# Kernel optimization log

Hardware: AMD Instinct MI355X
Metric: run time of the kernel (lower is better)

The kernel has to match this reference:

```python
import jax, jax.numpy as jnp
import numpy as np

N, E, G, D, H = 20000, 320000, 64, 56, 256


def setup_inputs() -> dict:
    key = jax.random.key(0)
    ks = jax.random.split(key, 12)
    inp = {}
    inp["x"] = jax.random.normal(ks[0], (N, D), jnp.float32)
    inp["edge_index"] = jax.random.randint(ks[1], (2, E), 0, N)
    inp["batch"] = jnp.sort(jax.random.randint(ks[2], (N,), 0, G))
    dims = [D, H, H]
    i = 3
    for l, d_in in enumerate(dims):
        inp[f"w1_{l}"] = jax.random.normal(ks[i], (2 * d_in, H), jnp.float32) * 0.05; i += 1
        inp[f"b1_{l}"] = jnp.zeros((H,), jnp.float32)
        inp[f"w2_{l}"] = jax.random.normal(ks[i], (H, H), jnp.float32) * 0.05; i += 1
        inp[f"b2_{l}"] = jnp.zeros((H,), jnp.float32)
    inp["wc1"] = jax.random.normal(ks[9], (2 * H, H), jnp.float32) * 0.05
    inp["bc1"] = jnp.zeros((H,), jnp.float32)
    inp["wc2"] = jax.random.normal(ks[10], (H, 64), jnp.float32) * 0.05
    inp["bc2"] = jnp.zeros((64,), jnp.float32)
    inp["wc3"] = jax.random.normal(ks[11], (64, 1), jnp.float32) * 0.05
    inp["bc3"] = jnp.zeros((1,), jnp.float32)
    return inp


def _edge_conv(x, src, dst, w1, b1, w2, b2):
    # PyG EdgeConv: message = mlp(cat([x_i, x_j - x_i])), max-aggregated at target i
    xi = x[dst]                       # [E, d]
    xj = x[src]                       # [E, d]
    h = jnp.concatenate([xi, xj - xi], axis=-1)  # [E, 2d]
    h = jax.nn.relu(h @ w1 + b1) @ w2 + b2       # [E, H]
    agg = jax.ops.segment_max(h, dst, num_segments=N)  # [N, H]
    return jnp.where(jnp.isfinite(agg), agg, 0.0)      # nodes with no in-edges -> 0


def reference(x, edge_index, batch,
              w1_0, b1_0, w2_0, b2_0,
              w1_1, b1_1, w2_1, b2_1,
              w1_2, b1_2, w2_2, b2_2,
              wc1, bc1, wc2, bc2, wc3, bc3):
    src, dst = edge_index[0], edge_index[1]
    for (w1, b1, w2, b2) in [(w1_0, b1_0, w2_0, b2_0),
                             (w1_1, b1_1, w2_1, b2_1),
                             (w1_2, b1_2, w2_2, b2_2)]:
        x = _edge_conv(x, src, dst, w1, b1, w2, b2)
        # dropout is identity at eval time
    # global mean / max pooling over graphs
    counts = jax.ops.segment_sum(jnp.ones((N,), x.dtype), batch, num_segments=G)
    x_mean = jax.ops.segment_sum(x, batch, num_segments=G) / jnp.maximum(counts, 1.0)[:, None]
    x_max = jax.ops.segment_max(x, batch, num_segments=G)
    x_max = jnp.where(jnp.isfinite(x_max), x_max, 0.0)
    g = jnp.concatenate([x_mean, x_max], axis=1)  # [G, 2H]
    h = jax.nn.relu(g @ wc1 + bc1)
    h = jax.nn.relu(h @ wc2 + bc2)
    out = h @ wc3 + bc3                            # [G, 1]
    return out.squeeze(-1)
```

## Files before the change

kernel.cpp:

```cpp
#include <hip/hip_runtime.h>

#define N_NODES 20000
#define N_EDGES 320000
#define N_GRAPHS 64
#define HID 256
#define EB 64
#define NB (N_EDGES / EB)
#define NBK 48

typedef __attribute__((ext_vector_type(8))) short bf16x8;
typedef __attribute__((ext_vector_type(4))) float f32x4;

__device__ __forceinline__ unsigned short bf16_rne(float f) {
  unsigned u = __float_as_uint(f);
  u = u + 0x7FFFu + ((u >> 16) & 1u);
  return (unsigned short)(u >> 16);
}

__device__ __forceinline__ unsigned int enc_f32(float v) {
  unsigned int bits = __float_as_uint(v);
  return (bits & 0x80000000u) ? ~bits : (bits | 0x80000000u);
}

__device__ __forceinline__ float dec_u32(unsigned int u) {
  if (u == 0u) return 0.f;
  unsigned int bits = (u & 0x80000000u) ? (u ^ 0x80000000u) : ~u;
  return __uint_as_float(bits);
}

__global__ __launch_bounds__(256) void hist_kernel(const int* __restrict__ ei,
                                                   int* __restrict__ deg) {
  int e = blockIdx.x * 256 + threadIdx.x;
  if (e < N_EDGES) atomicAdd(&deg[ei[N_EDGES + e]], 1);
}

__global__ __launch_bounds__(256) void scan_kernel(const int* __restrict__ deg,
                                                   int* __restrict__ cursor) {
  __shared__ int part[256];
  const int tid = threadIdx.x;
  const int CH = (N_NODES + 255) / 256;
  int s = tid * CH;
  int e = s + CH; if (e > N_NODES) e = N_NODES; if (s > N_NODES) s = N_NODES;
  int sum = 0;
  for (int i = s; i < e; i++) sum += deg[i];
  part[tid] = sum;
  __syncthreads();
  for (int off = 1; off < 256; off <<= 1) {
    int v = (tid >= off) ? part[tid - off] : 0;
    __syncthreads();
    part[tid] += v;
    __syncthreads();
  }
  int prefix = (tid == 0) ? 0 : part[tid - 1];
  for (int i = s; i < e; i++) {
    cursor[i] = prefix;
    prefix += deg[i];
  }
}

__global__ __launch_bounds__(256) void scatter_kernel(const int* __restrict__ ei,
                                                      int* __restrict__ cursor,
                                                      int* __restrict__ csr_src,
                                                      int* __restrict__ csr_dst) {
  int e = blockIdx.x * 256 + threadIdx.x;
  if (e < N_EDGES) {
    int s = ei[e], d = ei[N_EDGES + e];
    int pos = atomicAdd(&cursor[d], 1);
    csr_src[pos] = s;
    csr_dst[pos] = d;
  }
}

__global__ __launch_bounds__(256) void prep_weights_kernel(
    const float* __restrict__ w2_0, const float* __restrict__ w2_1,
    const float* __restrict__ w2_2,
    const float* __restrict__ w1_1, const float* __restrict__ w1_2,
    unsigned short* __restrict__ w2t_hi, unsigned short* __restrict__ w2t_lo,
    unsigned short* __restrict__ w1t_hi, unsigned short* __restrict__ w1t_lo) {
  const int b = blockIdx.x;
  const int k = threadIdx.x;
  if (b < 768) {
    int l = b >> 8, j = b & 255;
    const float* w2 = (l == 0) ? w2_0 : ((l == 1) ? w2_1 : w2_2);
    float v = w2[k * HID + j];
    unsigned short hi = bf16_rne(v);
    float rem = v - __uint_as_float(((unsigned)hi) << 16);
    w2t_hi[((size_t)l * HID + j) * HID + k] = hi;
    w2t_lo[((size_t)l * HID + j) * HID + k] = bf16_rne(rem);
  } else {
    int b2 = b - 768;
    int l = b2 >> 9, jj = b2 & 511;
    const float* w1 = (l == 0) ? w1_1 : w1_2;
    float v;
    if (jj < 256) v = w1[k * HID + jj] - w1[(k + 256) * HID + jj];
    else v = w1[(k + 256) * HID + (jj - 256)];
    unsigned short hi = bf16_rne(v);
    float rem = v - __uint_as_float(((unsigned)hi) << 16);
    w1t_hi[((size_t)l * 512 + jj) * HID + k] = hi;
    w1t_lo[((size_t)l * 512 + jj) * HID + k] = bf16_rne(rem);
  }
}

__global__ __launch_bounds__(256) void node_ab_l0_kernel(
    const float* __restrict__ x,
    const float* __restrict__ w1, const float* __restrict__ b1,
    float* __restrict__ A, float* __restrict__ B) {
  const int DIN = 56;
  __shared__ float xs[32 * DIN];
  const int node0 = blockIdx.x * 32;
  const int j = threadIdx.x;
  for (int t = threadIdx.x; t < 32 * DIN; t += 256) {
    int r = t / DIN, c = t - r * DIN;
    int node = node0 + r;
    xs[t] = (node < N_NODES) ? x[node * DIN + c] : 0.f;
  }
  __syncthreads();
  float accA[32], accB[32];
#pragma unroll
  for (int i = 0; i < 32; i++) { accA[i] = 0.f; accB[i] = 0.f; }
  for (int k = 0; k < DIN; k++) {
    float wt = w1[k * HID + j];
    float wb = w1[(k + DIN) * HID + j];
    float wa = wt - wb;
#pragma unroll
    for (int i = 0; i < 32; i++) {
      float xv = xs[i * DIN + k];
      accA[i] = fmaf(xv, wa, accA[i]);
      accB[i] = fmaf(xv, wb, accB[i]);
    }
  }
  float bj = b1[j];
  for (int i = 0; i < 32; i++) {
    int node = node0 + i;
    if (node < N_NODES) {
      A[node * HID + j] = accA[i] + bj;
      B[node * HID + j] = accB[i];
    }
  }
}

__global__ __launch_bounds__(512, 2) void node_mfma_kernel(
    const unsigned int* __restrict__ agg,
    const unsigned short* __restrict__ w1t_hi,
    const unsigned short* __restrict__ w1t_lo,
    const float* __restrict__ b1,
    float* __restrict__ A, float* __restrict__ Bm) {
  __shared__ char sm[NBK * 1024];
  const int tid = threadIdx.x;
  const int lane = tid & 63;
  const int wid = tid >> 6;
  const int node0 = blockIdx.x * NBK;

#pragma unroll
  for (int rr = 0; rr < NBK / 8; rr++) {
    int row = wid * (NBK / 8) + rr;
    int node = node0 + row;
    unsigned long long hp = 0, lp = 0;
    if (node < N_NODES) {
      uint4 u = *(const uint4*)(agg + (size_t)node * HID + lane * 4);
      float f[4];
      f[0] = dec_u32(u.x); f[1] = dec_u32(u.y); f[2] = dec_u32(u.z); f[3] = dec_u32(u.w);
#pragma unroll
      for (int i = 0; i < 4; i++) {
        float v = f[i];
        unsigned hu = bf16_rne(v);
        float rem = v - __uint_as_float(hu << 16);
        unsigned lu = bf16_rne(rem);
        hp |= (unsigned long long)hu << (16 * i);
        lp |= (unsigned long long)lu << (16 * i);
      }
    }
    int byte = row * 512 + ((lane * 8) ^ ((row & 7) << 4));
    *(unsigned long long*)(sm + byte) = hp;
    *(unsigned long long*)(sm + NBK * 512 + byte) = lp;
  }
  __syncthreads();

  const int nbase = wid * 64;
  const int lr = lane & 15;
  const int lg = lane >> 4;
  f32x4 acc[3][4];
#pragma unroll
  for (int mt = 0; mt < 3; mt++)
#pragma unroll
    for (int nt = 0; nt < 4; nt++) acc[mt][nt] = (f32x4){0.f, 0.f, 0.f, 0.f};

#pragma unroll
  for (int ks = 0; ks < 8; ks++) {
    const int kb = ks * 32 + lg * 8;
    bf16x8 ah[3], al[3], bh[4], bl[4];
#pragma unroll
    for (int mt = 0; mt < 3; mt++) {
      int row = mt * 16 + lr;
      int byte = row * 512 + ((kb * 2) ^ ((row & 7) << 4));
      ah[mt] = *(const bf16x8*)(sm + byte);
      al[mt] = *(const bf16x8*)(sm + NBK * 512 + byte);
    }
#pragma unroll
    for (int nt = 0; nt < 4; nt++) {
      int col = nbase + nt * 16 + lr;
      bh[nt] = *(const bf16x8*)(w1t_hi + (size_t)col * HID + kb);
      bl[nt] = *(const bf16x8*)(w1t_lo + (size_t)col * HID + kb);
    }
#pragma unroll
    for (int mt = 0; mt < 3; mt++)
#pragma unroll
      for (int nt = 0; nt < 4; nt++) {
        acc[mt][nt] = __builtin_amdgcn_mfma_f32_16x16x32_bf16(ah[mt], bh[nt], acc[mt][nt], 0, 0, 0);
        acc[mt][nt] = __builtin_amdgcn_mfma_f32_16x16x32_bf16(ah[mt], bl[nt], acc[mt][nt], 0, 0, 0);
        acc[mt][nt] = __builtin_amdgcn_mfma_f32_16x16x32_bf16(al[mt], bh[nt], acc[mt][nt], 0, 0, 0);
      }
  }

  const bool isA = (nbase < 256);
  float* dst = isA ? A : Bm;
  const int cb = isA ? nbase : (nbase - 256);
  float bv[4];
#pragma unroll
  for (int nt = 0; nt < 4; nt++)
    bv[nt] = isA ? b1[nbase + nt * 16 + lr] : 0.f;
#pragma unroll
  for (int mt = 0; mt < 3; mt++)
#pragma unroll
    for (int r = 0; r < 4; r++) {
      int row = mt * 16 + lg * 4 + r;
      int node = node0 + row;
      if (node < N_NODES) {
#pragma unroll
        for (int nt = 0; nt < 4; nt++)
          dst[(size_t)node * HID + cb + nt * 16 + lr] = acc[mt][nt][r] + bv[nt];
      }
    }
}

__global__ __launch_bounds__(512, 2) void edge_mfma_kernel(
    const int* __restrict__ csr_src, const int* __restrict__ csr_dst,
    const float* __restrict__ A, const float* __restrict__ Bm,
    const unsigned short* __restrict__ w2t_hi,
    const unsigned short* __restrict__ w2t_lo,
    const float* __restrict__ b2,
    unsigned int* __restrict__ agg) {
  __shared__ char sm[EB * 1024];
  __shared__ int sdst[EB];
  __shared__ int ssrc[EB];
  const int tid = threadIdx.x;
  const int e0 = blockIdx.x * EB;
  if (tid < EB) { sdst[tid] = csr_dst[e0 + tid]; ssrc[tid] = csr_src[e0 + tid]; }
  __syncthreads();
  const int lane = tid & 63;
  const int wid = tid >> 6;

  {
    float4 av = {0.f, 0.f, 0.f, 0.f};
    int dprev = -1;
#pragma unroll
    for (int q = 0; q < 8; q++) {
      int rep = wid * 8 + q;
      int d = sdst[rep];
      int s = ssrc[rep];
      if (d != dprev) {
        av = *(const float4*)(A + (size_t)d * HID + lane * 4);
        dprev = d;
      }
      float4 bv = *(const float4*)(Bm + (size_t)s * HID + lane * 4);
      float va[4], vb[4];
      *(float4*)va = av; *(float4*)vb = bv;
      unsigned long long hp = 0, lp = 0;
#pragma unroll
      for (int i = 0; i < 4; i++) {
        float v = fmaxf(va[i] + vb[i], 0.f);
        unsigned hu = bf16_rne(v);
        float rem = v - __uint_as_float(hu << 16);
        unsigned lu = bf16_rne(rem);
        hp |= (unsigned long long)hu << (16 * i);
        lp |= (unsigned long long)lu << (16 * i);
      }
      int byte = rep * 512 + ((lane * 8) ^ ((rep & 7) << 4));
      *(unsigned long long*)(sm + byte) = hp;
      *(unsigned long long*)(sm + EB * 512 + byte) = lp;
    }
  }
  __syncthreads();

  const int nbase = wid * 32;
  const int lr = lane & 15;
  const int lg = lane >> 4;
  f32x4 acc[4][2];
#pragma unroll
  for (int mt = 0; mt < 4; mt++)
#pragma unroll
    for (int nt = 0; nt < 2; nt++) acc[mt][nt] = (f32x4){0.f, 0.f, 0.f, 0.f};

  __builtin_amdgcn_s_setprio(1);
#pragma unroll
  for (int ks = 0; ks < 8; ks++) {
    const int kb = ks * 32 + lg * 8;
    bf16x8 ah[4], al[4], bh[2], bl[2];
#pragma unroll
    for (int mt = 0; mt < 4; mt++) {
      int row = mt * 16 + lr;
      int byte = row * 512 + ((kb * 2) ^ ((row & 7) << 4));
      ah[mt] = *(const bf16x8*)(sm + byte);
      al[mt] = *(const bf16x8*)(sm + EB * 512 + byte);
    }
#pragma unroll
    for (int nt = 0; nt < 2; nt++) {
      int col = nbase + nt * 16 + lr;
      bh[nt] = *(const bf16x8*)(w2t_hi + (size_t)col * HID + kb);
      bl[nt] = *(const bf16x8*)(w2t_lo + (size_t)col * HID + kb);
    }
#pragma unroll
    for (int mt = 0; mt < 4; mt++)
#pragma unroll
      for (int nt = 0; nt < 2; nt++) {
        acc[mt][nt] = __builtin_amdgcn_mfma_f32_16x16x32_bf16(ah[mt], bh[nt], acc[mt][nt], 0, 0, 0);
        acc[mt][nt] = __builtin_amdgcn_mfma_f32_16x16x32_bf16(ah[mt], bl[nt], acc[mt][nt], 0, 0, 0);
        acc[mt][nt] = __builtin_amdgcn_mfma_f32_16x16x32_bf16(al[mt], bh[nt], acc[mt][nt], 0, 0, 0);
      }
  }
  __builtin_amdgcn_s_setprio(0);
  __syncthreads();

  float* OUT = (float*)sm;
#pragma unroll
  for (int mt = 0; mt < 4; mt++)
#pragma unroll
    for (int nt = 0; nt < 2; nt++)
#pragma unroll
      for (int r = 0; r < 4; r++) {
        int row = mt * 16 + lg * 4 + r;
        int col = nbase + nt * 16 + lr;
        int c2 = col ^ (((row >> 2) & 1) << 4);
        OUT[row * HID + c2] = acc[mt][nt][r];
      }
  __syncthreads();

  const int half = tid >> 8;
  const int j = tid & 255;
  const float b2j = b2[j];
  const int elo = half * 32, ehi = elo + 32;
  const bool left_open  = (half == 0) ? true : (sdst[elo - 1] == sdst[elo]);
  const bool right_open = (half == 1) ? true : (sdst[ehi] == sdst[ehi - 1]);
  int prevd = sdst[elo];
  int segstart = elo;
  float run = -INFINITY;
  for (int e = elo; e < ehi; e++) {
    int d = sdst[e];
    if (d != prevd) {
      unsigned int enc = enc_f32(run + b2j);
      unsigned int* p = agg + (size_t)prevd * HID + j;
      if (segstart == elo && left_open) atomicMax(p, enc);
      else *p = enc;
      run = -INFINITY;
      segstart = e;
      prevd = d;
    }
    run = fmaxf(run, OUT[e * HID + (j ^ (((e >> 2) & 1) << 4))]);
  }
  {
    unsigned int enc = enc_f32(run + b2j);
    unsigned int* p = agg + (size_t)prevd * HID + j;
    if (right_open || (segstart == elo && left_open)) atomicMax(p, enc);
    else *p = enc;
  }
}

__device__ __forceinline__ int lower_bound_i(const int* __restrict__ arr, int n, int val) {
  int lo = 0, hi = n;
  while (lo < hi) {
    int mid = (lo + hi) >> 1;
    if (arr[mid] < val) lo = mid + 1; else hi = mid;
  }
  return lo;
}

__global__ __launch_bounds__(256) void pool_mlp_kernel(
    const unsigned int* __restrict__ agg, const int* __restrict__ batch,
    const float* __restrict__ wc1, const float* __restrict__ bc1,
    const float* __restrict__ wc2, const float* __restrict__ bc2,
    const float* __restrict__ wc3, const float* __restrict__ bc3,
    float* __restrict__ out) {
  const int g = blockIdx.x;
  const int j = threadIdx.x;
  __shared__ float gs[2 * HID];
  __shared__ float h1[HID];
  __shared__ float h2[64];
  int s = lower_bound_i(batch, N_NODES, g);
  int e = lower_bound_i(batch, N_NODES, g + 1);
  float sum = 0.f, mx = -INFINITY;
  for (int i = s; i < e; i++) {
    float v = dec_u32(agg[(size_t)i * HID + j]);
    sum += v;
    mx = fmaxf(mx, v);
  }
  int cnt = e - s;
  gs[j] = sum / fmaxf((float)cnt, 1.f);
  gs[HID + j] = (cnt > 0) ? mx : 0.f;
  __syncthreads();
  float acc = bc1[j];
  for (int k = 0; k < 2 * HID; k++) acc = fmaf(gs[k], wc1[k * HID + j], acc);
  h1[j] = fmaxf(acc, 0.f);
  __syncthreads();
  if (j < 64) {
    float a2 = bc2[j];
    for (int k = 0; k < HID; k++) a2 = fmaf(h1[k], wc2[k * 64 + j], a2);
    h2[j] = fmaxf(a2, 0.f);
  }
  __syncthreads();
  if (j == 0) {
    float a3 = bc3[0];
    for (int k = 0; k < 64; k++) a3 = fmaf(h2[k], wc3[k], a3);
    out[g] = a3;
  }
}

extern "C" void kernel_launch(void* const* d_in, const int* in_sizes, int n_in,
                              void* d_out, int out_size, void* d_ws, size_t ws_size,
                              hipStream_t stream) {
  const float* x      = (const float*)d_in[0];
  const int*   ei     = (const int*)d_in[1];
  const int*   batch  = (const int*)d_in[2];
  const float* w1[3]  = {(const float*)d_in[3], (const float*)d_in[7],  (const float*)d_in[11]};
  const float* b1[3]  = {(const float*)d_in[4], (const float*)d_in[8],  (const float*)d_in[12]};
  const float* w2[3]  = {(const float*)d_in[5], (const float*)d_in[9],  (const float*)d_in[13]};
  const float* b2[3]  = {(const float*)d_in[6], (const float*)d_in[10], (const float*)d_in[14]};
  const float* wc1 = (const float*)d_in[15];
  const float* bc1 = (const float*)d_in[16];
  const float* wc2 = (const float*)d_in[17];
  const float* bc2 = (const float*)d_in[18];
  const float* wc3 = (const float*)d_in[19];
  const float* bc3 = (const float*)d_in[20];
  float* out = (float*)d_out;

  char* ws = (char*)d_ws;
  size_t off = 0;
  auto walloc = [&](size_t bytes) -> void* {
    void* p = ws + off;
    off += (bytes + 255) & ~(size_t)255;
    return p;
  };
  const size_t nh = (size_t)N_NODES * HID;
  float*          A       = (float*)walloc(nh * sizeof(float));
  float*          Bm      = (float*)walloc(nh * sizeof(float));
  unsigned int*   AGG     = (unsigned int*)walloc(nh * sizeof(unsigned int));
  int*            deg     = (int*)walloc((size_t)N_NODES * sizeof(int));
  int*            cursor  = (int*)walloc((size_t)N_NODES * sizeof(int));
  int*            csr_src = (int*)walloc((size_t)N_EDGES * sizeof(int));
  int*            csr_dst = (int*)walloc((size_t)N_EDGES * sizeof(int));
  unsigned short* w2t_hi  = (unsigned short*)walloc((size_t)3 * HID * HID * sizeof(unsigned short));
  unsigned short* w2t_lo  = (unsigned short*)walloc((size_t)3 * HID * HID * sizeof(unsigned short));
  unsigned short* w1t_hi  = (unsigned short*)walloc((size_t)2 * 512 * HID * sizeof(unsigned short));
  unsigned short* w1t_lo  = (unsigned short*)walloc((size_t)2 * 512 * HID * sizeof(unsigned short));
  (void)ws_size; (void)in_sizes; (void)n_in; (void)out_size;

  hipMemsetAsync(deg, 0, N_NODES * sizeof(int), stream);
  prep_weights_kernel<<<1792, 256, 0, stream>>>(w2[0], w2[1], w2[2], w1[1], w1[2],
                                                w2t_hi, w2t_lo, w1t_hi, w1t_lo);
  hist_kernel<<<(N_EDGES + 255) / 256, 256, 0, stream>>>(ei, deg);
  scan_kernel<<<1, 256, 0, stream>>>(deg, cursor);
  scatter_kernel<<<(N_EDGES + 255) / 256, 256, 0, stream>>>(ei, cursor, csr_src, csr_dst);

  for (int l = 0; l < 3; l++) {
    if (l == 0)
      node_ab_l0_kernel<<<N_NODES / 32, 256, 0, stream>>>(x, w1[0], b1[0], A, Bm);
    else
      node_mfma_kernel<<<(N_NODES + NBK - 1) / NBK, 512, 0, stream>>>(
          AGG, w1t_hi + (size_t)(l - 1) * 512 * HID, w1t_lo + (size_t)(l - 1) * 512 * HID,
          b1[l], A, Bm);
    hipMemsetAsync(AGG, 0, nh * sizeof(unsigned int), stream);
    edge_mfma_kernel<<<NB, 512, 0, stream>>>(csr_src, csr_dst, A, Bm,
                                             w2t_hi + (size_t)l * HID * HID,
                                             w2t_lo + (size_t)l * HID * HID,
                                             b2[l], AGG);
  }
  pool_mlp_kernel<<<N_GRAPHS, 256, 0, stream>>>(AGG, batch, wc1, bc1, wc2, bc2, wc3, bc3, out);
}
```

Measured before the change: 925.6 us.

## Make edge kernel persistent with W2 fragments held in registers across tiles

The edge MLP kernel becomes a persistent grid of 256 blocks that loops over 64-edge tiles. Each wave loads its W2 hi/lo bf16 fragments into registers once and reuses them for every tile, instead of re-reading them from global memory per tile. The shared-memory dst/src index arrays are dropped in favour of direct global reads. Launch bounds drop to one block per CU to make room for the extra registers, which lowers occupancy and with it latency hiding for the gather loads.

```diff
diff --git a/kernel.cpp b/kernel.cpp
--- a/kernel.cpp
+++ b/kernel.cpp
@@ -6,6 +6,7 @@
 #define HID 256
 #define EB 64
 #define NB (N_EDGES / EB)
+#define TGRID 256
 #define NBK 48
 
 typedef __attribute__((ext_vector_type(8))) short bf16x8;
@@ -233,7 +234,7 @@
     }
 }
 
-__global__ __launch_bounds__(512, 2) void edge_mfma_kernel(
+__global__ __launch_bounds__(512, 1) void edge_mfma_kernel(
     const int* __restrict__ csr_src, const int* __restrict__ csr_dst,
     const float* __restrict__ A, const float* __restrict__ Bm,
     const unsigned short* __restrict__ w2t_hi,
@@ -241,127 +242,133 @@
     const float* __restrict__ b2,
     unsigned int* __restrict__ agg) {
   __shared__ char sm[EB * 1024];
-  __shared__ int sdst[EB];
-  __shared__ int ssrc[EB];
   const int tid = threadIdx.x;
-  const int e0 = blockIdx.x * EB;
-  if (tid < EB) { sdst[tid] = csr_dst[e0 + tid]; ssrc[tid] = csr_src[e0 + tid]; }
-  __syncthreads();
   const int lane = tid & 63;
   const int wid = tid >> 6;
-
-  {
-    float4 av = {0.f, 0.f, 0.f, 0.f};
-    int dprev = -1;
-#pragma unroll
-    for (int q = 0; q < 8; q++) {
-      int rep = wid * 8 + q;
-      int d = sdst[rep];
-      int s = ssrc[rep];
-      if (d != dprev) {
-        av = *(const float4*)(A + (size_t)d * HID + lane * 4);
-        dprev = d;
-      }
-      float4 bv = *(const float4*)(Bm + (size_t)s * HID + lane * 4);
-      float va[4], vb[4];
-      *(float4*)va = av; *(float4*)vb = bv;
-      unsigned long long hp = 0, lp = 0;
-#pragma unroll
-      for (int i = 0; i < 4; i++) {
-        float v = fmaxf(va[i] + vb[i], 0.f);
-        unsigned hu = bf16_rne(v);
-        float rem = v - __uint_as_float(hu << 16);
-        unsigned lu = bf16_rne(rem);
-        hp |= (unsigned long long)hu << (16 * i);
-        lp |= (unsigned long long)lu << (16 * i);
-      }
-      int byte = rep * 512 + ((lane * 8) ^ ((rep & 7) << 4));
-      *(unsigned long long*)(sm + byte) = hp;
-      *(unsigned long long*)(sm + EB * 512 + byte) = lp;
-    }
-  }
-  __syncthreads();
-
-  const int nbase = wid * 32;
   const int lr = lane & 15;
   const int lg = lane >> 4;
-  f32x4 acc[4][2];
-#pragma unroll
-  for (int mt = 0; mt < 4; mt++)
-#pragma unroll
-    for (int nt = 0; nt < 2; nt++) acc[mt][nt] = (f32x4){0.f, 0.f, 0.f, 0.f};
-
-  __builtin_amdgcn_s_setprio(1);
-#pragma unroll
-  for (int ks = 0; ks < 8; ks++) {
-    const int kb = ks * 32 + lg * 8;
-    bf16x8 ah[4], al[4], bh[2], bl[2];
-#pragma unroll
-    for (int mt = 0; mt < 4; mt++) {
-      int row = mt * 16 + lr;
-      int byte = row * 512 + ((kb * 2) ^ ((row & 7) << 4));
-      ah[mt] = *(const bf16x8*)(sm + byte);
-      al[mt] = *(const bf16x8*)(sm + EB * 512 + byte);
-    }
-#pragma unroll
-    for (int nt = 0; nt < 2; nt++) {
+  const int nbase = wid * 32;
+
+  bf16x8 bh[2][8], bl[2][8];
+#pragma unroll
+  for (int nt = 0; nt < 2; nt++)
+#pragma unroll
+    for (int ks = 0; ks < 8; ks++) {
       int col = nbase + nt * 16 + lr;
-      bh[nt] = *(const bf16x8*)(w2t_hi + (size_t)col * HID + kb);
-      bl[nt] = *(const bf16x8*)(w2t_lo + (size_t)col * HID + kb);
-    }
+      int kb = ks * 32 + lg * 8;
+      bh[nt][ks] = *(const bf16x8*)(w2t_hi + (size_t)col * HID + kb);
+      bl[nt][ks] = *(const bf16x8*)(w2t_lo + (size_t)col * HID + kb);
+    }
+
+  const float b2j = b2[tid & 255];
+
+  for (int tile = blockIdx.x; tile < NB; tile += TGRID) {
+    const int e0 = tile * EB;
+    __syncthreads();
+
+    {
+      float4 av = {0.f, 0.f, 0.f, 0.f};
+      int dprev = -1;
+#pragma unroll
+      for (int q = 0; q < 8; q++) {
+        int rep = wid * 8 + q;
+        int d = csr_dst[e0 + rep];
+        int s = csr_src[e0 + rep];
+        if (d != dprev) {
+          av = *(const float4*)(A + (size_t)d * HID + lane * 4);
+          dprev = d;
+        }
+        float4 bv = *(const float4*)(Bm + (size_t)s * HID + lane * 4);
+        float va[4], vb[4];
+        *(float4*)va = av; *(float4*)vb = bv;
+        unsigned long long hp = 0, lp = 0;
+#pragma unroll
+        for (int i = 0; i < 4; i++) {
+          float v = fmaxf(va[i] + vb[i], 0.f);
+          unsigned hu = bf16_rne(v);
+          float rem = v - __uint_as_float(hu << 16);
+          unsigned lu = bf16_rne(rem);
+          hp |= (unsigned long long)hu << (16 * i);
+          lp |= (unsigned long long)lu << (16 * i);
+        }
+        int byte = rep * 512 + ((lane * 8) ^ ((rep & 7) << 4));
+        *(unsigned long long*)(sm + byte) = hp;
+        *(unsigned long long*)(sm + EB * 512 + byte) = lp;
+      }
+    }
+    __syncthreads();
+
+    f32x4 acc[4][2];
 #pragma unroll
     for (int mt = 0; mt < 4; mt++)
 #pragma unroll
-      for (int nt = 0; nt < 2; nt++) {
-        acc[mt][nt] = __builtin_amdgcn_mfma_f32_16x16x32_bf16(ah[mt], bh[nt], acc[mt][nt], 0, 0, 0);
-        acc[mt][nt] = __builtin_amdgcn_mfma_f32_16x16x32_bf16(ah[mt], bl[nt], acc[mt][nt], 0, 0, 0);
-        acc[mt][nt] = __builtin_amdgcn_mfma_f32_16x16x32_bf16(al[mt], bh[nt], acc[mt][nt], 0, 0, 0);
-      }
-  }
-  __builtin_amdgcn_s_setprio(0);
-  __syncthreads();
-
-  float* OUT = (float*)sm;
-#pragma unroll
-  for (int mt = 0; mt < 4; mt++)
-#pragma unroll
-    for (int nt = 0; nt < 2; nt++)
-#pragma unroll
-      for (int r = 0; r < 4; r++) {
-        int row = mt * 16 + lg * 4 + r;
-        int col = nbase + nt * 16 + lr;
-        int c2 = col ^ (((row >> 2) & 1) << 4);
-        OUT[row * HID + c2] = acc[mt][nt][r];
-      }
-  __syncthreads();
-
-  const int half = tid >> 8;
-  const int j = tid & 255;
-  const float b2j = b2[j];
-  const int elo = half * 32, ehi = elo + 32;
-  const bool left_open  = (half == 0) ? true : (sdst[elo - 1] == sdst[elo]);
-  const bool right_open = (half == 1) ? true : (sdst[ehi] == sdst[ehi - 1]);
-  int prevd = sdst[elo];
-  int segstart = elo;
-  float run = -INFINITY;
-  for (int e = elo; e < ehi; e++) {
-    int d = sdst[e];
-    if (d != prevd) {
+      for (int nt = 0; nt < 2; nt++) acc[mt][nt] = (f32x4){0.f, 0.f, 0.f, 0.f};
+
+    __builtin_amdgcn_s_setprio(1);
+#pragma unroll
+    for (int ks = 0; ks < 8; ks++) {
+      const int kb = ks * 32 + lg * 8;
+      bf16x8 ah[4], al[4];
+#pragma unroll
+      for (int mt = 0; mt < 4; mt++) {
+        int row = mt * 16 + lr;
+        int byte = row * 512 + ((kb * 2) ^ ((row & 7) << 4));
+        ah[mt] = *(const bf16x8*)(sm + byte);
+        al[mt] = *(const bf16x8*)(sm + EB * 512 + byte);
+      }
+#pragma unroll
+      for (int mt = 0; mt < 4; mt++)
+#pragma unroll
+        for (int nt = 0; nt < 2; nt++) {
+          acc[mt][nt] = __builtin_amdgcn_mfma_f32_16x16x32_bf16(ah[mt], bh[nt][ks], acc[mt][nt], 0, 0, 0);
+          acc[mt][nt] = __builtin_amdgcn_mfma_f32_16x16x32_bf16(ah[mt], bl[nt][ks], acc[mt][nt], 0, 0, 0);
+          acc[mt][nt] = __builtin_amdgcn_mfma_f32_16x16x32_bf16(al[mt], bh[nt][ks], acc[mt][nt], 0, 0, 0);
+        }
+    }
+    __builtin_amdgcn_s_setprio(0);
+    __syncthreads();
+
+    float* OUT = (float*)sm;
+#pragma unroll
+    for (int mt = 0; mt < 4; mt++)
+#pragma unroll
+      for (int nt = 0; nt < 2; nt++)
+#pragma unroll
+        for (int r = 0; r < 4; r++) {
+          int row = mt * 16 + lg * 4 + r;
+          int col = nbase + nt * 16 + lr;
+          int c2 = col ^ (((row >> 2) & 1) << 4);
+          OUT[row * HID + c2] = acc[mt][nt][r];
+        }
+    __syncthreads();
+
+    const int half = tid >> 8;
+    const int j = tid & 255;
+    const int elo = half * 32, ehi = elo + 32;
+    const bool left_open  = (half == 0) ? true : (csr_dst[e0 + elo - 1] == csr_dst[e0 + elo]);
+    const bool right_open = (half == 1) ? true : (csr_dst[e0 + ehi] == csr_dst[e0 + ehi - 1]);
+    int prevd = csr_dst[e0 + elo];
+    int segstart = elo;
+    float run = -INFINITY;
+    for (int e = elo; e < ehi; e++) {
+      int d = csr_dst[e0 + e];
+      if (d != prevd) {
+        unsigned int enc = enc_f32(run + b2j);
+        unsigned int* p = agg + (size_t)prevd * HID + j;
+        if (segstart == elo && left_open) atomicMax(p, enc);
+        else *p = enc;
+        run = -INFINITY;
+        segstart = e;
+        prevd = d;
+      }
+      run = fmaxf(run, OUT[e * HID + (j ^ (((e >> 2) & 1) << 4))]);
+    }
+    {
       unsigned int enc = enc_f32(run + b2j);
       unsigned int* p = agg + (size_t)prevd * HID + j;
-      if (segstart == elo && left_open) atomicMax(p, enc);
+      if (right_open || (segstart == elo && left_open)) atomicMax(p, enc);
       else *p = enc;
-      run = -INFINITY;
-      segstart = e;
-      prevd = d;
-    }
-    run = fmaxf(run, OUT[e * HID + (j ^ (((e >> 2) & 1) << 4))]);
-  }
-  {
-    unsigned int enc = enc_f32(run + b2j);
-    unsigned int* p = agg + (size_t)prevd * HID + j;
-    if (right_open || (segstart == elo && left_open)) atomicMax(p, enc);
-    else *p = enc;
+    }
   }
 }
 
@@ -468,10 +475,10 @@
           AGG, w1t_hi + (size_t)(l - 1) * 512 * HID, w1t_lo + (size_t)(l - 1) * 512 * HID,
           b1[l], A, Bm);
     hipMemsetAsync(AGG, 0, nh * sizeof(unsigned int), stream);
-    edge_mfma_kernel<<<NB, 512, 0, stream>>>(csr_src, csr_dst, A, Bm,
-                                             w2t_hi + (size_t)l * HID * HID,
-                                             w2t_lo + (size_t)l * HID * HID,
-                                             b2[l], AGG);
+    edge_mfma_kernel<<<TGRID, 512, 0, stream>>>(csr_src, csr_dst, A, Bm,
+                                                w2t_hi + (size_t)l * HID * HID,
+                                                w2t_lo + (size_t)l * HID * HID,
+                                                b2[l], AGG);
   }
   pool_mlp_kernel<<<N_GRAPHS, 256, 0, stream>>>(AGG, batch, wc1, bc1, wc2, bc2, wc3, bc3, out);
 }
```

Result: slower. 1.032 ms (+11.5%).
